# Kernel optimization log

Hardware: AMD Instinct MI355X
Metric: run time of the kernel (lower is better)

The kernel has to match this reference:

```python
import jax, jax.numpy as jnp
import numpy as np

B, T, N_AGENTS = 256, 200, 8
OBS_DIM, OUT_DIM, RNN_IN, RNN_H = 128, 16, 64, 64
IN_DIM = OBS_DIM + N_AGENTS  # 136


def setup_inputs() -> dict:
    key = jax.random.key(0)
    ks = jax.random.split(key, 8)
    def lin(k, fan_out, fan_in):
        bound = 1.0 / np.sqrt(fan_in)
        return jax.random.uniform(k, (fan_out, fan_in), jnp.float32, -bound, bound)
    obs_history = jax.random.normal(ks[0], (B, T, N_AGENTS, OBS_DIM), jnp.float32)
    # agent id per slot n, constant over batch/time (ids 0..N_AGENTS-1)
    agent = jnp.broadcast_to(jnp.arange(N_AGENTS, dtype=jnp.int32)[None, None, :, None],
                             (B, T, N_AGENTS, 1))
    return {
        "obs_history": obs_history,
        "agent": agent,
        "W1": lin(ks[1], RNN_IN, IN_DIM),
        "b1": jnp.zeros((RNN_IN,), jnp.float32),
        "W_ih": lin(ks[2], 3 * RNN_H, RNN_IN),
        "W_hh": lin(ks[3], 3 * RNN_H, RNN_H),
        "b_ih": jnp.zeros((3 * RNN_H,), jnp.float32),
        "b_hh": jnp.zeros((3 * RNN_H,), jnp.float32),
        "W2": lin(ks[4], OUT_DIM, RNN_H),
        "b2": jnp.zeros((OUT_DIM,), jnp.float32),
    }


def _drqn_scan(x, W1, b1, W_ih, W_hh, b_ih, b_hh, W2, b2):
    # x: [T, BN, IN_DIM]
    def step(h, xt):
        a = jax.nn.relu(xt @ W1.T + b1)                 # fc1: [BN, RNN_IN]
        gi = a @ W_ih.T + b_ih                          # [BN, 3H]
        gh = h @ W_hh.T + b_hh                          # [BN, 3H]
        i_r, i_z, i_n = jnp.split(gi, 3, axis=-1)
        h_r, h_z, h_n = jnp.split(gh, 3, axis=-1)
        r = jax.nn.sigmoid(i_r + h_r)
        z = jax.nn.sigmoid(i_z + h_z)
        n = jnp.tanh(i_n + r * h_n)
        h_new = (1.0 - z) * n + z * h                   # GRUCell update
        q = h_new @ W2.T + b2                           # fc2: [BN, OUT]
        return h_new, q
    h0 = jnp.zeros((x.shape[1], RNN_H), x.dtype)
    _, qs = jax.lax.scan(step, h0, x)
    return qs  # [T, BN, OUT]


def reference(obs_history, agent, W1, b1, W_ih, W_hh, b_ih, b_hh, W2, b2):
    # agent id per slot n (constant over batch/time): agent[0,...,n,:].max()
    agent_ids = jnp.max(agent[0, :, :, 0], axis=0)                 # [N]
    oh = jax.nn.one_hot(agent_ids, N_AGENTS, dtype=obs_history.dtype)  # [N, N_AGENTS]
    oh_b = jnp.broadcast_to(oh[None, None], (B, T, N_AGENTS, N_AGENTS))
    x = jnp.concatenate([obs_history, oh_b], axis=-1)              # [B,T,N,IN]
    x = jnp.transpose(x, (1, 0, 2, 3)).reshape(T, B * N_AGENTS, IN_DIM)
    qs = _drqn_scan(x, W1, b1, W_ih, W_hh, b_ih, b_hh, W2, b2)     # [T,BN,OUT]
    nn_output = jnp.transpose(qs.reshape(T, B, N_AGENTS, OUT_DIM), (1, 0, 2, 3))
    # per-agent max over that agent's valid action dim (all = OUT_DIM here)
    action_dims = [OUT_DIM] * N_AGENTS
    max_values = jnp.stack(
        [jnp.max(nn_output[..., n, :action_dims[n]], axis=-1) for n in range(N_AGENTS)], axis=-1)
    max_actions = jnp.stack(
        [jnp.argmax(nn_output[..., n, :action_dims[n]], axis=-1) for n in range(N_AGENTS)],
        axis=-1).astype(jnp.float32)
    return nn_output, max_values, max_actions
```

## Files before the change

kernel.cpp:

```cpp
#include <hip/hip_runtime.h>


namespace {
constexpr int kB = 256, kT = 200, kN = 8, kObs = 128, kH = 64, kOut = 16;
constexpr int kRows = kB * kT * kN;
constexpr size_t kABytes  = (size_t)kRows * 64 * 4;
constexpr size_t kGiBytes = (size_t)kRows * 192 * 4;
}

__global__ __launch_bounds__(256, 2)
void fc1_k(const float* __restrict__ obs, const int* __restrict__ agent,
           const float* __restrict__ W1, const float* __restrict__ b1,
           float* __restrict__ a_out) {
  __shared__ float xs[2][2][128];
  __shared__ float ps[2][2][64];
  __shared__ float ohs[512];
  const int tid = threadIdx.x, lane = tid & 63, w = tid >> 6;
  const int e = w >> 1, p = w & 1;

  for (int i = tid; i < 512; i += 256) {
    int n = i >> 6, l = i & 63;
    ohs[i] = W1[(size_t)l * 136 + 128 + agent[n]];
  }

  float4 wv[16];
  #pragma unroll
  for (int k = 0; k < 16; ++k)
    wv[k] = *(const float4*)(W1 + (size_t)lane * 136 + p * 64 + k * 4);
  const float b1r = b1[lane];

  constexpr int ROWS = 100;
  const int eng = blockIdx.x * 2 + e;
  const int r0 = eng * ROWS;
  const int et = p * 64 + lane;

  xs[e][0][et] = obs[(size_t)r0 * 128 + et];
  float xq = obs[(size_t)(r0 + 1) * 128 + et];
  __syncthreads();

  #pragma unroll 1
  for (int i = 0; i < ROWS; ++i) {
    const int r = r0 + i;
    if (i + 1 < ROWS) xs[e][(i + 1) & 1][et] = xq;
    const int nr = (i + 2 < ROWS) ? (r0 + i + 2) : (r0 + ROWS - 1);
    xq = obs[(size_t)nr * 128 + et];

    const float* xb = xs[e][i & 1] + p * 64;
    float a0 = 0.f, a1 = 0.f, a2 = 0.f, a3 = 0.f;
    #pragma unroll
    for (int k = 0; k < 16; ++k) {
      float4 xp = *(const float4*)(xb + k * 4);
      a0 = fmaf(wv[k].x, xp.x, a0);
      a1 = fmaf(wv[k].y, xp.y, a1);
      a2 = fmaf(wv[k].z, xp.z, a2);
      a3 = fmaf(wv[k].w, xp.w, a3);
    }
    const float part = (a0 + a1) + (a2 + a3);
    if (p == 0) ps[e][i & 1][lane] = part;
    __syncthreads();
    if (p == 1) {
      float av = part + ps[e][i & 1][lane] + b1r + ohs[(r & 7) * 64 + lane];
      a_out[(size_t)r * 64 + lane] = fmaxf(av, 0.f);
    }
  }
}

__global__ __launch_bounds__(256, 2)
void gi_k(const float* __restrict__ a_glob, const float* __restrict__ Wih,
          const float* __restrict__ bih, float* __restrict__ gi_out) {
  __shared__ float as_[4][2][64];
  const int tid = threadIdx.x, lane = tid & 63, w = tid >> 6;

  float wir[64], wiz[64], win_[64];
  #pragma unroll
  for (int k = 0; k < 64; k += 4) {
    *(float4*)&wir[k]  = *(const float4*)(Wih + (size_t)lane * 64 + k);
    *(float4*)&wiz[k]  = *(const float4*)(Wih + (size_t)(64 + lane) * 64 + k);
    *(float4*)&win_[k] = *(const float4*)(Wih + (size_t)(128 + lane) * 64 + k);
  }
  const float bir = bih[lane], biz = bih[64 + lane], bin_ = bih[128 + lane];

  const int gwave = blockIdx.x * 4 + w;
  const int r0 = gwave * 200;
  float (*ab)[64] = as_[w];

  ab[0][lane] = a_glob[(size_t)r0 * 64 + lane];
  float qA = a_glob[(size_t)(r0 + 1) * 64 + lane];
  float qB = a_glob[(size_t)(r0 + 2) * 64 + lane];

#define GI_BODY(T, Q, NEXT)                                                    \
  {                                                                            \
    const int t_ = (T);                                                        \
    if (t_ < 199) ab[(t_ + 1) & 1][lane] = Q;                                  \
    const int nr_ = (NEXT) > 199 ? 199 : (NEXT);                               \
    Q = a_glob[(size_t)(r0 + nr_) * 64 + lane];                                \
    const float* ap_ = ab[t_ & 1];                                             \
    float r0a = bir, r1a = 0.f, z0a = biz, z1a = 0.f, n0a = bin_, n1a = 0.f;   \
    _Pragma("unroll") for (int k = 0; k < 64; k += 4) {                        \
      float4 av = *(const float4*)(ap_ + k);                                   \
      r0a = fmaf(wir[k], av.x, r0a);  r1a = fmaf(wir[k + 1], av.y, r1a);       \
      r0a = fmaf(wir[k + 2], av.z, r0a); r1a = fmaf(wir[k + 3], av.w, r1a);    \
      z0a = fmaf(wiz[k], av.x, z0a);  z1a = fmaf(wiz[k + 1], av.y, z1a);       \
      z0a = fmaf(wiz[k + 2], av.z, z0a); z1a = fmaf(wiz[k + 3], av.w, z1a);    \
      n0a = fmaf(win_[k], av.x, n0a); n1a = fmaf(win_[k + 1], av.y, n1a);      \
      n0a = fmaf(win_[k + 2], av.z, n0a); n1a = fmaf(win_[k + 3], av.w, n1a);  \
    }                                                                          \
    float* gp_ = gi_out + (size_t)(r0 + t_) * 192;                             \
    gp_[lane] = r0a + r1a;                                                     \
    gp_[64 + lane] = z0a + z1a;                                                \
    gp_[128 + lane] = n0a + n1a;                                               \
  }

  #pragma unroll 1
  for (int i = 0; i < 200; i += 2) {
    GI_BODY(i + 0, qA, i + 3)
    GI_BODY(i + 1, qB, i + 4)
  }
#undef GI_BODY
}

__global__ __launch_bounds__(64, 1)
void gru3_k(const float* __restrict__ gi_glob,
            const float* __restrict__ Whh, const float* __restrict__ bhh,
            const float* __restrict__ W2, const float* __restrict__ b2,
            float* __restrict__ out) {
  __shared__ float hs[64];
  const int lane = threadIdx.x;

  float whr[64], whz[64], whn[64];
  #pragma unroll
  for (int k = 0; k < 64; k += 4) {
    *(float4*)&whr[k] = *(const float4*)(Whh + (size_t)lane * 64 + k);
    *(float4*)&whz[k] = *(const float4*)(Whh + (size_t)(64 + lane) * 64 + k);
    *(float4*)&whn[k] = *(const float4*)(Whh + (size_t)(128 + lane) * 64 + k);
  }
  const float bhr = bhh[lane], bhz = bhh[64 + lane], bhn = bhh[128 + lane];
  const int m = lane & 15, qt = lane >> 4;
  float w2r[16];
  #pragma unroll
  for (int j = 0; j < 16; j += 4)
    *(float4*)&w2r[j] = *(const float4*)(W2 + (size_t)m * 64 + qt * 16 + j);
  const float b2r = b2[m];

  const int s = blockIdx.x;
  const int b = s >> 3, n = s & 7;
  const size_t rbase = (size_t)b * 1600 + n;

  float* outq  = out;
  float* outmv = out + (size_t)kRows * 16;
  float* outma = outmv + kRows;

  hs[lane] = 0.f;
  float h = 0.f;

  const float* gp0 = gi_glob + rbase * 192;
  float gA0 = gp0[lane], gA1 = gp0[64 + lane], gA2 = gp0[128 + lane];
  const float* gp1 = gi_glob + (rbase + 8) * 192;
  float gB0 = gp1[lane], gB1 = gp1[64 + lane], gB2 = gp1[128 + lane];

#define GRU_STEP(T, G0, G1, G2, TN)                                            \
  {                                                                            \
    const int t_ = (T);                                                        \
    const size_t r_ = rbase + (size_t)t_ * 8;                                  \
    float hr0 = bhr, hr1 = 0.f, hz0 = bhz, hz1 = 0.f, hn0 = bhn, hn1 = 0.f;    \
    _Pragma("unroll") for (int k = 0; k < 64; k += 4) {                        \
      float4 hp = *(const float4*)(hs + k);                                    \
      hr0 = fmaf(whr[k], hp.x, hr0);  hr1 = fmaf(whr[k + 1], hp.y, hr1);       \
      hr0 = fmaf(whr[k + 2], hp.z, hr0); hr1 = fmaf(whr[k + 3], hp.w, hr1);    \
      hz0 = fmaf(whz[k], hp.x, hz0);  hz1 = fmaf(whz[k + 1], hp.y, hz1);       \
      hz0 = fmaf(whz[k + 2], hp.z, hz0); hz1 = fmaf(whz[k + 3], hp.w, hz1);    \
      hn0 = fmaf(whn[k], hp.x, hn0);  hn1 = fmaf(whn[k + 1], hp.y, hn1);       \
      hn0 = fmaf(whn[k + 2], hp.z, hn0); hn1 = fmaf(whn[k + 3], hp.w, hn1);    \
    }                                                                          \
    const float rg = 1.f / (1.f + __expf(-((G0) + hr0 + hr1)));                \
    const float zg = 1.f / (1.f + __expf(-((G1) + hz0 + hz1)));                \
    const float e2 = __expf(2.f * ((G2) + rg * (hn0 + hn1)));                  \
    const float ng = 1.f - 2.f / (e2 + 1.f);                                   \
    h = (1.f - zg) * ng + zg * h;                                              \
    hs[lane] = h;                                                              \
    const int tn_ = (TN) > 199 ? 199 : (TN);                                   \
    const float* gp_ = gi_glob + (rbase + (size_t)tn_ * 8) * 192;              \
    G0 = gp_[lane]; G1 = gp_[64 + lane]; G2 = gp_[128 + lane];                 \
    float q0 = 0.f, q1 = 0.f;                                                  \
    _Pragma("unroll") for (int j = 0; j < 16; j += 4) {                        \
      float4 hp = *(const float4*)(hs + qt * 16 + j);                          \
      q0 = fmaf(w2r[j], hp.x, q0);     q1 = fmaf(w2r[j + 1], hp.y, q1);        \
      q0 = fmaf(w2r[j + 2], hp.z, q0); q1 = fmaf(w2r[j + 3], hp.w, q1);        \
    }                                                                          \
    float q = q0 + q1;                                                         \
    q += __shfl_xor(q, 16);                                                    \
    q += __shfl_xor(q, 32);                                                    \
    q += b2r;                                                                  \
    if (lane < 16) outq[r_ * 16 + m] = q;                                      \
    float bv = q; int bi = m;                                                  \
    _Pragma("unroll") for (int d = 1; d < 16; d <<= 1) {                       \
      float ov = __shfl_xor(bv, d, 16);                                        \
      int oi = __shfl_xor(bi, d, 16);                                          \
      if (ov > bv || (ov == bv && oi < bi)) { bv = ov; bi = oi; }              \
    }                                                                          \
    if (lane == 0) { outmv[r_] = bv; outma[r_] = (float)bi; }                  \
  }

  #pragma unroll 1
  for (int t = 0; t < 200; t += 2) {
    GRU_STEP(t, gA0, gA1, gA2, t + 2)
    GRU_STEP(t + 1, gB0, gB1, gB2, t + 3)
  }
#undef GRU_STEP
}

namespace fb {
constexpr int kW1Pitch = 137, kHPitch = 65;
constexpr int OFF_W1 = 0;
constexpr int OFF_WIH = OFF_W1 + 64 * kW1Pitch;
constexpr int OFF_WHH = OFF_WIH + 192 * kHPitch;
constexpr int OFF_W2 = OFF_WHH + 192 * kHPitch;
constexpr int OFF_B1 = OFF_W2 + 16 * kHPitch;
constexpr int OFF_BIH = OFF_B1 + 64;
constexpr int OFF_BHH = OFF_BIH + 192;
constexpr int OFF_B2 = OFF_BHH + 192;
constexpr int LDS_FLOATS = OFF_B2 + 16;
}

__device__ __forceinline__ float bcastf(float v, int l) {
  return __int_as_float(__builtin_amdgcn_readlane(__float_as_int(v), l));
}

__global__ __launch_bounds__(512, 1)
void drqn_fused(const float* __restrict__ obs, const int* __restrict__ agent,
                const float* __restrict__ W1, const float* __restrict__ b1,
                const float* __restrict__ Wih, const float* __restrict__ Whh,
                const float* __restrict__ bih, const float* __restrict__ bhh,
                const float* __restrict__ W2, const float* __restrict__ b2,
                float* __restrict__ out) {
  using namespace fb;
  extern __shared__ float lds[];
  float* W1s = lds + OFF_W1; float* Wihs = lds + OFF_WIH;
  float* Whhs = lds + OFF_WHH; float* W2s = lds + OFF_W2;
  float* b1s = lds + OFF_B1; float* bihs = lds + OFF_BIH;
  float* bhhs = lds + OFF_BHH; float* b2s = lds + OFF_B2;
  const int tid = threadIdx.x;
  for (int i = tid; i < 64 * 136; i += 512) { int r = i / 136, c = i - r * 136; W1s[r * kW1Pitch + c] = W1[i]; }
  for (int i = tid; i < 192 * 64; i += 512) { int r = i >> 6, c = i & 63; Wihs[r * kHPitch + c] = Wih[i]; }
  for (int i = tid; i < 192 * 64; i += 512) { int r = i >> 6, c = i & 63; Whhs[r * kHPitch + c] = Whh[i]; }
  for (int i = tid; i < 16 * 64; i += 512) { int r = i >> 6, c = i & 63; W2s[r * kHPitch + c] = W2[i]; }
  if (tid < 64) b1s[tid] = b1[tid];
  if (tid < 192) bihs[tid] = bih[tid];
  if (tid < 192) bhhs[tid] = bhh[tid];
  if (tid < 16) b2s[tid] = b2[tid];
  __syncthreads();
  const int wave = tid >> 6, lane = tid & 63;
  const int s = blockIdx.x * 8 + wave;
  const int b = s >> 3, n = s & 7;
  const int acol = 128 + agent[n];
  const float* obase = obs + (((size_t)b * kT) * kN + n) * kObs;
  const size_t qbase = (((size_t)b * kT) * kN + n) * kOut;
  const size_t mbase = ((size_t)b * kT) * kN + n;
  float* outq = out;
  float* outmv = out + (size_t)kB * kT * kN * kOut;
  float* outma = outmv + (size_t)kB * kT * kN;
  float h = 0.f;
  float xa = obase[lane], xb = obase[64 + lane];
  #pragma unroll 1
  for (int t = 0; t < kT; ++t) {
    float xan = 0.f, xbn = 0.f;
    if (t + 1 < kT) { const float* p = obase + (size_t)(t + 1) * kN * kObs; xan = p[lane]; xbn = p[64 + lane]; }
    float acc = b1s[lane] + W1s[lane * kW1Pitch + acol];
    #pragma unroll
    for (int k = 0; k < 64; ++k) acc += W1s[lane * kW1Pitch + k] * bcastf(xa, k);
    #pragma unroll
    for (int k = 0; k < 64; ++k) acc += W1s[lane * kW1Pitch + 64 + k] * bcastf(xb, k);
    float a = fmaxf(acc, 0.f);
    float air = bihs[lane], aiz = bihs[64 + lane], ain = bihs[128 + lane];
    #pragma unroll
    for (int k = 0; k < 64; ++k) {
      float sa = bcastf(a, k);
      air += Wihs[lane * kHPitch + k] * sa;
      aiz += Wihs[(64 + lane) * kHPitch + k] * sa;
      ain += Wihs[(128 + lane) * kHPitch + k] * sa;
    }
    float ghr = bhhs[lane], ghz = bhhs[64 + lane], ghn = bhhs[128 + lane];
    #pragma unroll
    for (int k = 0; k < 64; ++k) {
      float sh = bcastf(h, k);
      ghr += Whhs[lane * kHPitch + k] * sh;
      ghz += Whhs[(64 + lane) * kHPitch + k] * sh;
      ghn += Whhs[(128 + lane) * kHPitch + k] * sh;
    }
    float rg = 1.f / (1.f + expf(-(air + ghr)));
    float zg = 1.f / (1.f + expf(-(aiz + ghz)));
    float ng = tanhf(ain + rg * ghn);
    h = (1.f - zg) * ng + zg * h;
    const int m = lane & 15;
    float q = b2s[m];
    #pragma unroll
    for (int k = 0; k < 64; ++k) q += W2s[m * kHPitch + k] * bcastf(h, k);
    if (lane < 16) outq[qbase + (size_t)t * kN * kOut + m] = q;
    float bv = q; int bi = m;
    #pragma unroll
    for (int d = 1; d < 16; d <<= 1) {
      float ov = __shfl_xor(bv, d, 16);
      int oi = __shfl_xor(bi, d, 16);
      if (ov > bv || (ov == bv && oi < bi)) { bv = ov; bi = oi; }
    }
    if (lane == 0) { outmv[mbase + (size_t)t * kN] = bv; outma[mbase + (size_t)t * kN] = (float)bi; }
    xa = xan; xb = xbn;
  }
}

extern "C" void kernel_launch(void* const* d_in, const int* in_sizes, int n_in,
                              void* d_out, int out_size, void* d_ws, size_t ws_size,
                              hipStream_t stream) {
  const float* obs  = (const float*)d_in[0];
  const int* agent  = (const int*)d_in[1];
  const float* W1   = (const float*)d_in[2];
  const float* b1   = (const float*)d_in[3];
  const float* Wih  = (const float*)d_in[4];
  const float* Whh  = (const float*)d_in[5];
  const float* bih  = (const float*)d_in[6];
  const float* bhh  = (const float*)d_in[7];
  const float* W2   = (const float*)d_in[8];
  const float* b2   = (const float*)d_in[9];
  float* out = (float*)d_out;

  if (ws_size >= kABytes + kGiBytes) {
    float* a_buf  = (float*)d_ws;
    float* gi_buf = (float*)((char*)d_ws + kABytes);
    fc1_k<<<dim3(2048), dim3(256), 0, stream>>>(obs, agent, W1, b1, a_buf);
    gi_k<<<dim3(512), dim3(256), 0, stream>>>(a_buf, Wih, bih, gi_buf);
    gru3_k<<<dim3(2048), dim3(64), 0, stream>>>(gi_buf, Whh, bhh, W2, b2, out);
  } else {
    (void)hipFuncSetAttribute((const void*)drqn_fused,
                              hipFuncAttributeMaxDynamicSharedMemorySize,
                              fb::LDS_FLOATS * 4);
    drqn_fused<<<dim3(256), dim3(512), fb::LDS_FLOATS * 4, stream>>>(
        obs, agent, W1, b1, Wih, Whh, bih, bhh, W2, b2, out);
  }
}
```

Baseline: 595.8 us.

## Split GRU recurrence K-dimension across two waves with LDS partial-sum exchange

The recurrent GRU kernel now runs two wavefronts per sequence. Each wave holds half of the W_hh columns in registers and computes partial gate dot products, and the partials are combined through shared memory with barriers. Wave 1 then does the gate math, the fc2 projection and the argmax. This halves the serial FMA chain per step and register pressure, allowing higher occupancy, but adds two block barriers per timestep. W2 is now reloaded from global memory each step instead of being held in registers.

```diff
diff --git a/kernel.cpp b/kernel.cpp
--- a/kernel.cpp
+++ b/kernel.cpp
@@ -119,94 +119,106 @@
 #undef GI_BODY
 }
 
-__global__ __launch_bounds__(64, 1)
-void gru3_k(const float* __restrict__ gi_glob,
+__global__ __launch_bounds__(128, 2)
+void gru7_k(const float* __restrict__ gi_glob,
             const float* __restrict__ Whh, const float* __restrict__ bhh,
             const float* __restrict__ W2, const float* __restrict__ b2,
             float* __restrict__ out) {
   __shared__ float hs[64];
-  const int lane = threadIdx.x;
-
-  float whr[64], whz[64], whn[64];
+  __shared__ float ps[3][64];
+  const int tid = threadIdx.x, lane = tid & 63, p = tid >> 6;
+
+  float wr[32], wz[32], wn[32];
   #pragma unroll
-  for (int k = 0; k < 64; k += 4) {
-    *(float4*)&whr[k] = *(const float4*)(Whh + (size_t)lane * 64 + k);
-    *(float4*)&whz[k] = *(const float4*)(Whh + (size_t)(64 + lane) * 64 + k);
-    *(float4*)&whn[k] = *(const float4*)(Whh + (size_t)(128 + lane) * 64 + k);
+  for (int k = 0; k < 32; k += 4) {
+    *(float4*)&wr[k] = *(const float4*)(Whh + (size_t)lane * 64 + p * 32 + k);
+    *(float4*)&wz[k] = *(const float4*)(Whh + (size_t)(64 + lane) * 64 + p * 32 + k);
+    *(float4*)&wn[k] = *(const float4*)(Whh + (size_t)(128 + lane) * 64 + p * 32 + k);
   }
   const float bhr = bhh[lane], bhz = bhh[64 + lane], bhn = bhh[128 + lane];
   const int m = lane & 15, qt = lane >> 4;
-  float w2r[16];
-  #pragma unroll
-  for (int j = 0; j < 16; j += 4)
-    *(float4*)&w2r[j] = *(const float4*)(W2 + (size_t)m * 64 + qt * 16 + j);
-  const float b2r = b2[m];
 
   const int s = blockIdx.x;
-  const int b = s >> 3, n = s & 7;
-  const size_t rbase = (size_t)b * 1600 + n;
+  const size_t rbase = (size_t)(s >> 3) * 1600 + (s & 7);
 
   float* outq  = out;
   float* outmv = out + (size_t)kRows * 16;
   float* outma = outmv + kRows;
 
-  hs[lane] = 0.f;
   float h = 0.f;
-
-  const float* gp0 = gi_glob + rbase * 192;
-  float gA0 = gp0[lane], gA1 = gp0[64 + lane], gA2 = gp0[128 + lane];
-  const float* gp1 = gi_glob + (rbase + 8) * 192;
-  float gB0 = gp1[lane], gB1 = gp1[64 + lane], gB2 = gp1[128 + lane];
-
-#define GRU_STEP(T, G0, G1, G2, TN)                                            \
+  if (p == 0) hs[lane] = 0.f;
+
+  float gA0 = 0.f, gA1 = 0.f, gA2 = 0.f, gB0 = 0.f, gB1 = 0.f, gB2 = 0.f;
+  if (p == 1) {
+    const float* g0 = gi_glob + rbase * 192;
+    gA0 = g0[lane]; gA1 = g0[64 + lane]; gA2 = g0[128 + lane];
+    const float* g1 = gi_glob + (rbase + 8) * 192;
+    gB0 = g1[lane]; gB1 = g1[64 + lane]; gB2 = g1[128 + lane];
+  }
+  __syncthreads();
+
+#define G7_STEP(T, G0, G1, G2, TN)                                             \
   {                                                                            \
-    const int t_ = (T);                                                        \
-    const size_t r_ = rbase + (size_t)t_ * 8;                                  \
-    float hr0 = bhr, hr1 = 0.f, hz0 = bhz, hz1 = 0.f, hn0 = bhn, hn1 = 0.f;    \
-    _Pragma("unroll") for (int k = 0; k < 64; k += 4) {                        \
-      float4 hp = *(const float4*)(hs + k);                                    \
-      hr0 = fmaf(whr[k], hp.x, hr0);  hr1 = fmaf(whr[k + 1], hp.y, hr1);       \
-      hr0 = fmaf(whr[k + 2], hp.z, hr0); hr1 = fmaf(whr[k + 3], hp.w, hr1);    \
-      hz0 = fmaf(whz[k], hp.x, hz0);  hz1 = fmaf(whz[k + 1], hp.y, hz1);       \
-      hz0 = fmaf(whz[k + 2], hp.z, hz0); hz1 = fmaf(whz[k + 3], hp.w, hz1);    \
-      hn0 = fmaf(whn[k], hp.x, hn0);  hn1 = fmaf(whn[k + 1], hp.y, hn1);       \
-      hn0 = fmaf(whn[k + 2], hp.z, hn0); hn1 = fmaf(whn[k + 3], hp.w, hn1);    \
+                        \
+    const float* hb_ = hs + p * 32;                                            \
+    float ar = 0.f, az = 0.f, an = 0.f;                                        \
+    _Pragma("unroll") for (int k = 0; k < 32; k += 4) {                        \
+      float4 hv = *(const float4*)(hb_ + k);               \
+      ar = fmaf(wr[k], hv.x, ar);     az = fmaf(wz[k], hv.x, az);              \
+      an = fmaf(wn[k], hv.x, an);                                              \
+      ar = fmaf(wr[k + 1], hv.y, ar); az = fmaf(wz[k + 1], hv.y, az);          \
+      an = fmaf(wn[k + 1], hv.y, an);                                          \
+      ar = fmaf(wr[k + 2], hv.z, ar); az = fmaf(wz[k + 2], hv.z, az);          \
+      an = fmaf(wn[k + 2], hv.z, an);                                          \
+      ar = fmaf(wr[k + 3], hv.w, ar); az = fmaf(wz[k + 3], hv.w, az);          \
+      an = fmaf(wn[k + 3], hv.w, an);                                          \
     }                                                                          \
-    const float rg = 1.f / (1.f + __expf(-((G0) + hr0 + hr1)));                \
-    const float zg = 1.f / (1.f + __expf(-((G1) + hz0 + hz1)));                \
-    const float e2 = __expf(2.f * ((G2) + rg * (hn0 + hn1)));                  \
-    const float ng = 1.f - 2.f / (e2 + 1.f);                                   \
-    h = (1.f - zg) * ng + zg * h;                                              \
-    hs[lane] = h;                                                              \
-    const int tn_ = (TN) > 199 ? 199 : (TN);                                   \
-    const float* gp_ = gi_glob + (rbase + (size_t)tn_ * 8) * 192;              \
-    G0 = gp_[lane]; G1 = gp_[64 + lane]; G2 = gp_[128 + lane];                 \
-    float q0 = 0.f, q1 = 0.f;                                                  \
-    _Pragma("unroll") for (int j = 0; j < 16; j += 4) {                        \
-      float4 hp = *(const float4*)(hs + qt * 16 + j);                          \
-      q0 = fmaf(w2r[j], hp.x, q0);     q1 = fmaf(w2r[j + 1], hp.y, q1);        \
-      q0 = fmaf(w2r[j + 2], hp.z, q0); q1 = fmaf(w2r[j + 3], hp.w, q1);        \
+    if (p == 0) { ps[0][lane] = ar; ps[1][lane] = az; ps[2][lane] = an; }      \
+    __syncthreads();                                  \
+    if (p == 1) {                                                              \
+      const size_t r_ = rbase + (size_t)(T) * 8;                               \
+      const float ghr = ar + ps[0][lane] + bhr;                                \
+      const float ghz = az + ps[1][lane] + bhz;                                \
+      const float ghn = an + ps[2][lane] + bhn;                                \
+      const float rg = 1.f / (1.f + __expf(-((G0) + ghr)));                    \
+      const float zg = 1.f / (1.f + __expf(-((G1) + ghz)));                    \
+      const float e2 = __expf(2.f * ((G2) + rg * ghn));                        \
+      const float ng = 1.f - 2.f / (e2 + 1.f);                       \
+      h = (1.f - zg) * ng + zg * h;                                            \
+      hs[lane] = h;                                       \
+      const int tn_ = (TN) > 199 ? 199 : (TN);                                 \
+      const float* gp_ = gi_glob + (rbase + (size_t)tn_ * 8) * 192;            \
+      G0 = gp_[lane]; G1 = gp_[64 + lane]; G2 = gp_[128 + lane];               \
+                  \
+      float q0 = 0.f, q1 = 0.f;                                                \
+      _Pragma("unroll") for (int j = 0; j < 16; j += 4) {                      \
+        float4 hv = *(const float4*)(hs + qt * 16 + j);                        \
+        float4 wv = *(const float4*)(W2 + (size_t)m * 64 + qt * 16 + j);       \
+        q0 = fmaf(wv.x, hv.x, q0); q1 = fmaf(wv.y, hv.y, q1);                  \
+        q0 = fmaf(wv.z, hv.z, q0); q1 = fmaf(wv.w, hv.w, q1);                  \
+      }                                                                        \
+      float q = q0 + q1;                                                       \
+      q += __shfl_xor(q, 16);                                                  \
+      q += __shfl_xor(q, 32);                                                  \
+      q += b2[m];                                                              \
+      if (lane < 16) outq[r_ * 16 + m] = q;                                    \
+      float bv = q; int bi = m;                                                \
+      _Pragma("unroll") for (int d = 1; d < 16; d <<= 1) {                     \
+        float ov = __shfl_xor(bv, d, 16);                                      \
+        int oi = __shfl_xor(bi, d, 16);                                        \
+        if (ov > bv || (ov == bv && oi < bi)) { bv = ov; bi = oi; }            \
+      }                                                                        \
+      if (lane == 0) { outmv[r_] = bv; outma[r_] = (float)bi; }                \
     }                                                                          \
-    float q = q0 + q1;                                                         \
-    q += __shfl_xor(q, 16);                                                    \
-    q += __shfl_xor(q, 32);                                                    \
-    q += b2r;                                                                  \
-    if (lane < 16) outq[r_ * 16 + m] = q;                                      \
-    float bv = q; int bi = m;                                                  \
-    _Pragma("unroll") for (int d = 1; d < 16; d <<= 1) {                       \
-      float ov = __shfl_xor(bv, d, 16);                                        \
-      int oi = __shfl_xor(bi, d, 16);                                          \
-      if (ov > bv || (ov == bv && oi < bi)) { bv = ov; bi = oi; }              \
-    }                                                                          \
-    if (lane == 0) { outmv[r_] = bv; outma[r_] = (float)bi; }                  \
+    __syncthreads();                                    \
   }
 
   #pragma unroll 1
   for (int t = 0; t < 200; t += 2) {
-    GRU_STEP(t, gA0, gA1, gA2, t + 2)
-    GRU_STEP(t + 1, gB0, gB1, gB2, t + 3)
-  }
-#undef GRU_STEP
+    G7_STEP(t,     gA0, gA1, gA2, t + 2)
+    G7_STEP(t + 1, gB0, gB1, gB2, t + 3)
+  }
+#undef G7_STEP
 }
 
 namespace fb {
@@ -326,9 +338,9 @@
   if (ws_size >= kABytes + kGiBytes) {
     float* a_buf  = (float*)d_ws;
     float* gi_buf = (float*)((char*)d_ws + kABytes);
-    fc1_k<<<dim3(2048), dim3(256), 0, stream>>>(obs, agent, W1, b1, a_buf);
-    gi_k<<<dim3(512), dim3(256), 0, stream>>>(a_buf, Wih, bih, gi_buf);
-    gru3_k<<<dim3(2048), dim3(64), 0, stream>>>(gi_buf, Whh, bhh, W2, b2, out);
+    fc1_k <<<dim3(2048), dim3(256), 0, stream>>>(obs, agent, W1, b1, a_buf);
+    gi_k  <<<dim3(512), dim3(256), 0, stream>>>(a_buf, Wih, bih, gi_buf);
+    gru7_k<<<dim3(2048), dim3(128), 0, stream>>>(gi_buf, Whh, bhh, W2, b2, out);
   } else {
     (void)hipFuncSetAttribute((const void*)drqn_fused,
                               hipFuncAttributeMaxDynamicSharedMemorySize,
```

Result: slower. 844.2 us (+41.7%).
